# Kernel tuning notes

Hardware: AMD Instinct MI355X
Metric: run time of the kernel (lower is better)

The kernel has to match this reference:

```python
import jax, jax.numpy as jnp
import numpy as np

B, D, C, P, H, I, E, TOPK = 65536, 1024, 256, 32, 128, 32, 16, 2
FUSION = D + P  # 1056

def ln(x, g, b, eps=1e-5):
    m = jnp.mean(x, axis=-1, keepdims=True)
    v = jnp.mean((x - m) ** 2, axis=-1, keepdims=True)
    return (x - m) * jax.lax.rsqrt(v + eps) * g + b

def setup_inputs() -> dict:
    key = jax.random.key(0)
    ks = jax.random.split(key, 8)
    def w(k, shape):
        return jax.random.normal(k, shape, dtype=jnp.float32) * 0.02
    return {
        "x": jax.random.normal(ks[0], (B, D), dtype=jnp.float32),
        "context": jax.random.normal(ks[1], (B, C), dtype=jnp.float32),
        "en_g": jnp.ones((D,), jnp.float32), "en_b": jnp.zeros((D,), jnp.float32),
        "cn_g": jnp.ones((C,), jnp.float32), "cn_b": jnp.zeros((C,), jnp.float32),
        "cp1_w": w(ks[2], (C, P)), "cp1_b": jnp.zeros((P,), jnp.float32),
        "cp2_w": w(ks[3], (P, P)), "cp2_b": jnp.zeros((P,), jnp.float32),
        "cpn_g": jnp.ones((P,), jnp.float32), "cpn_b": jnp.zeros((P,), jnp.float32),
        "fn_g": jnp.ones((FUSION,), jnp.float32), "fn_b": jnp.zeros((FUSION,), jnp.float32),
        "gp1_w": w(ks[4], (FUSION, H)), "gp1_b": jnp.zeros((H,), jnp.float32),
        "ln1_g": jnp.ones((H,), jnp.float32), "ln1_b": jnp.zeros((H,), jnp.float32),
        "gp2_w": w(ks[5], (H, I)), "gp2_b": jnp.zeros((I,), jnp.float32),
        "ln2_g": jnp.ones((I,), jnp.float32), "ln2_b": jnp.zeros((I,), jnp.float32),
        "gp3_w": w(ks[6], (I, E)), "gp3_b": jnp.zeros((E,), jnp.float32),
    }

def reference(x, context, en_g, en_b, cn_g, cn_b, cp1_w, cp1_b, cp2_w, cp2_b,
              cpn_g, cpn_b, fn_g, fn_b, gp1_w, gp1_b, ln1_g, ln1_b,
              gp2_w, gp2_b, ln2_g, ln2_b, gp3_w, gp3_b):
    gelu = lambda t: jax.nn.gelu(t, approximate=False)  # torch default GELU (erf)
    emb = ln(x, en_g, en_b)                               # [B, D]
    ctx = ln(context, cn_g, cn_b)                         # [B, C]
    cf = gelu(ctx @ cp1_w + cp1_b) @ cp2_w + cp2_b        # [B, P]
    cf = ln(cf, cpn_g, cpn_b)
    fusion = ln(jnp.concatenate([emb, cf], axis=-1), fn_g, fn_b)  # [B, FUSION]
    h = gelu(ln(fusion @ gp1_w + gp1_b, ln1_g, ln1_b))    # [B, H]
    inter = gelu(ln(h @ gp2_w + gp2_b, ln2_g, ln2_b))     # [B, I]
    clean_logits = inter @ gp3_w + gp3_b                  # [B, E]
    # inference path: no noise injection (training=False)
    top_v, top_i = jax.lax.top_k(clean_logits, TOPK)
    combined_weights = jax.nn.softmax(top_v / 1.0, axis=-1)  # temperature=1.0
    return combined_weights, top_i, clean_logits
```

## Files before the change

### kernel.cpp

```cpp
#include <hip/hip_runtime.h>
#include <math.h>

namespace {

using s8v = __attribute__((ext_vector_type(8))) short;
using vf4 = __attribute__((ext_vector_type(4))) float;

constexpr int Bn = 65536;
constexpr int Rn = 64;

constexpr size_t OFF_A1H  = 0;
constexpr size_t OFF_A1M  = 270336;
constexpr size_t OFF_A1L  = 540672;
constexpr size_t OFF_C1H  = 811008;
constexpr size_t OFF_C1M  = 827392;
constexpr size_t OFF_C1L  = 843776;
constexpr size_t OFF_C2H  = 860160;
constexpr size_t OFF_C2M  = 862208;
constexpr size_t OFF_C2L  = 864256;
constexpr size_t OFF_G2H  = 866304;
constexpr size_t OFF_G2M  = 874496;
constexpr size_t OFF_G2L  = 882688;
constexpr size_t OFF_VPK  = 890880;
constexpr size_t OFF_UPK  = 892928;
constexpr size_t OFF_CST  = 893184;
constexpr size_t OFF_VPART= 893216;

__device__ __forceinline__ unsigned short bf16_rn(float f) {
    unsigned u = __float_as_uint(f);
    u += 0x7FFFu + ((u >> 16) & 1u);
    return (unsigned short)(u >> 16);
}
__device__ __forceinline__ float bf16_tof(unsigned short h) {
    return __uint_as_float(((unsigned)h) << 16);
}

union S8U { s8v v; unsigned short u[8]; };
union S8P { s8v v; unsigned u32[4]; };

__device__ __forceinline__ vf4 MFMA(s8v a, s8v b, vf4 c) {
    return __builtin_amdgcn_mfma_f32_16x16x32_bf16(a, b, c, 0, 0, 0);
}

__device__ __forceinline__ void mfma6(vf4& acc, s8v ah, s8v am, s8v al,
                                      s8v bh, s8v bm, s8v bl) {
    acc = MFMA(ah, bh, acc);
    acc = MFMA(ah, bm, acc);
    acc = MFMA(am, bh, acc);
    acc = MFMA(ah, bl, acc);
    acc = MFMA(al, bh, acc);
    acc = MFMA(am, bm, acc);
}

__device__ __forceinline__ void split3(float v, unsigned short& h,
                                       unsigned short& m, unsigned short& l) {
    h = bf16_rn(v);
    const float r = v - bf16_tof(h);
    m = bf16_rn(r);
    const float r2 = r - bf16_tof(m);
    l = bf16_rn(r2);
}

__device__ __forceinline__ void split3x8(const float* vv, s8v& H, s8v& M, s8v& L) {
    S8P h, m, l;
    #pragma unroll
    for (int p = 0; p < 4; ++p) {
        const float lo = vv[2 * p], hi = vv[2 * p + 1];
        unsigned ph, pm, pl;
        asm("v_cvt_pk_bf16_f32 %0, %1, %2" : "=v"(ph) : "v"(lo), "v"(hi));
        const float rlo = lo - __uint_as_float(ph << 16);
        const float rhi = hi - __uint_as_float(ph & 0xFFFF0000u);
        asm("v_cvt_pk_bf16_f32 %0, %1, %2" : "=v"(pm) : "v"(rlo), "v"(rhi));
        const float slo = rlo - __uint_as_float(pm << 16);
        const float shi = rhi - __uint_as_float(pm & 0xFFFF0000u);
        asm("v_cvt_pk_bf16_f32 %0, %1, %2" : "=v"(pl) : "v"(slo), "v"(shi));
        h.u32[p] = ph; m.u32[p] = pm; l.u32[p] = pl;
    }
    H = h.v; M = m.v; L = l.v;
}

__device__ __forceinline__ float gelu_f(float v) {
    return 0.5f * v * (1.0f + erff(v * 0.70710678118654752440f));
}

__device__ __forceinline__ void red16(float& s) {
    s += __shfl_xor(s, 1, 64); s += __shfl_xor(s, 2, 64);
    s += __shfl_xor(s, 4, 64); s += __shfl_xor(s, 8, 64);
}

__global__ void cag_prek1(const float* __restrict__ gp1_w,
                          const float* __restrict__ en_g, const float* __restrict__ en_b,
                          const float* __restrict__ fn_g, const float* __restrict__ fn_b,
                          char* __restrict__ ws)
{
    const int t = threadIdx.x, ch = blockIdx.x;
    s8v* A1h = (s8v*)(ws + OFF_A1H);
    s8v* A1m = (s8v*)(ws + OFF_A1M);
    s8v* A1l = (s8v*)(ws + OFF_A1L);
    float* Vpart = (float*)(ws + OFF_VPART);

    for (int s = t; s < 512; s += 256) {
        const int nt = s >> 6, lane = s & 63;
        const int n = nt * 16 + (lane & 15);
        const int jb = ch * 32 + 8 * (lane >> 4);
        S8U h, m, lo;
        #pragma unroll
        for (int r = 0; r < 8; ++r) {
            const int j = jb + r;
            const float sc = fn_g[j] * (j < 1024 ? en_g[j] : 1.0f);
            const float a = sc * gp1_w[(size_t)j * 128 + n];
            split3(a, h.u[r], m.u[r], lo.u[r]);
        }
        A1h[(ch * 8 + nt) * 64 + lane] = h.v;
        A1m[(ch * 8 + nt) * 64 + lane] = m.v;
        A1l[(ch * 8 + nt) * 64 + lane] = lo.v;
    }
    if (t < 128) {
        float v1 = 0.f, v2 = 0.f, v3 = 0.f, v4 = 0.f;
        for (int jj = 0; jj < 32; ++jj) {
            const int j = ch * 32 + jj;
            const float wv = gp1_w[(size_t)j * 128 + t];
            const float fg = fn_g[j];
            if (j < 1024) { v1 = fmaf(fg * en_g[j], wv, v1); v2 = fmaf(fg * en_b[j], wv, v2); }
            v3 = fmaf(fg, wv, v3);
            v4 = fmaf(fn_b[j], wv, v4);
        }
        float* p = Vpart + ((size_t)ch * 128 + t) * 4;
        p[0] = v1; p[1] = v2; p[2] = v3; p[3] = v4;
    }
}

__global__ void cag_prek2(const float* __restrict__ en_g, const float* __restrict__ en_b,
                          const float* __restrict__ cn_g, const float* __restrict__ cn_b,
                          const float* __restrict__ cp1_w, const float* __restrict__ cp1_b,
                          const float* __restrict__ cp2_w, const float* __restrict__ gp2_w,
                          const float* __restrict__ gp1_b,
                          char* __restrict__ ws)
{
    const int t = threadIdx.x, b = blockIdx.x;
    if (b == 0) {
        const float* Vpart = (const float*)(ws + OFF_VPART);
        float* Vpk = (float*)(ws + OFF_VPK);
        float* cst = (float*)(ws + OFF_CST);
        if (t < 128) {
            float v1 = 0.f, v2 = 0.f, v3 = 0.f, v4 = 0.f;
            for (int ch = 0; ch < 33; ++ch) {
                const float* p = Vpart + ((size_t)ch * 128 + t) * 4;
                v1 += p[0]; v2 += p[1]; v3 += p[2]; v4 += p[3];
            }
            v4 += gp1_b[t];
            float* q = Vpk + t * 4;
            q[0] = v1; q[1] = v2; q[2] = v3; q[3] = v4;
        }
        __shared__ float red[256];
        float part[5] = {0.f, 0.f, 0.f, 0.f, 0.f};
        for (int i = t; i < 1024; i += 256) {
            const float g = en_g[i], bb = en_b[i];
            part[0] += g; part[1] += bb; part[2] += g * g; part[3] += g * bb; part[4] += bb * bb;
        }
        for (int f = 0; f < 5; ++f) {
            red[t] = part[f]; __syncthreads();
            for (int s = 128; s > 0; s >>= 1) { if (t < s) red[t] += red[t + s]; __syncthreads(); }
            if (t == 0) cst[f] = red[0];
            __syncthreads();
        }
    } else if (b == 1) {
        s8v* C1h = (s8v*)(ws + OFF_C1H);
        s8v* C1m = (s8v*)(ws + OFF_C1M);
        s8v* C1l = (s8v*)(ws + OFF_C1L);
        float* up = (float*)(ws + OFF_UPK);
        for (int s = t; s < 8 * 2 * 64; s += 256) {
            const int ks = s >> 7, nt = (s >> 6) & 1, lane = s & 63;
            const int n = nt * 16 + (lane & 15);
            const int kb = ks * 32 + 8 * (lane >> 4);
            S8U h, m, lo;
            #pragma unroll
            for (int r = 0; r < 8; ++r) {
                const int k = kb + r;
                const float a = cn_g[k] * cp1_w[k * 32 + n];
                split3(a, h.u[r], m.u[r], lo.u[r]);
            }
            C1h[(ks * 2 + nt) * 64 + lane] = h.v;
            C1m[(ks * 2 + nt) * 64 + lane] = m.v;
            C1l[(ks * 2 + nt) * 64 + lane] = lo.v;
        }
        if (t < 32) {
            float u1 = 0.f, u2 = 0.f;
            for (int c = 0; c < 256; ++c) {
                u1 = fmaf(cn_g[c], cp1_w[c * 32 + t], u1);
                u2 = fmaf(cn_b[c], cp1_w[c * 32 + t], u2);
            }
            up[2 * t] = u1; up[2 * t + 1] = u2 + cp1_b[t];
        }
    } else if (b == 2) {
        s8v* C2h = (s8v*)(ws + OFF_C2H);
        s8v* C2m = (s8v*)(ws + OFF_C2M);
        s8v* C2l = (s8v*)(ws + OFF_C2L);
        if (t < 128) {
            const int nt = t >> 6, lane = t & 63;
            const int n = nt * 16 + (lane & 15);
            const int kb = 8 * (lane >> 4);
            S8U h, m, lo;
            #pragma unroll
            for (int r = 0; r < 8; ++r) {
                const float a = cp2_w[(kb + r) * 32 + n];
                split3(a, h.u[r], m.u[r], lo.u[r]);
            }
            C2h[nt * 64 + lane] = h.v;
            C2m[nt * 64 + lane] = m.v;
            C2l[nt * 64 + lane] = lo.v;
        }
    } else {
        s8v* G2h = (s8v*)(ws + OFF_G2H);
        s8v* G2m = (s8v*)(ws + OFF_G2M);
        s8v* G2l = (s8v*)(ws + OFF_G2L);
        for (int s = t; s < 4 * 2 * 64; s += 256) {
            const int ks = s >> 7, nt = (s >> 6) & 1, lane = s & 63;
            const int n = nt * 16 + (lane & 15);
            const int kb = ks * 32 + 8 * (lane >> 4);
            S8U h, m, lo;
            #pragma unroll
            for (int r = 0; r < 8; ++r) {
                const float a = gp2_w[(kb + r) * 32 + n];
                split3(a, h.u[r], m.u[r], lo.u[r]);
            }
            G2h[(ks * 2 + nt) * 64 + lane] = h.v;
            G2m[(ks * 2 + nt) * 64 + lane] = m.v;
            G2l[(ks * 2 + nt) * 64 + lane] = lo.v;
        }
    }
}

__global__ __launch_bounds__(256, 4)
void cag_main(const float* __restrict__ x, const float* __restrict__ ctx,
              const float* __restrict__ en_g, const float* __restrict__ en_b,
              const float* __restrict__ cpn_g, const float* __restrict__ cpn_b,
              const float* __restrict__ cp2_b,
              const float* __restrict__ ln1_g, const float* __restrict__ ln1_b,
              const float* __restrict__ gp2_b,
              const float* __restrict__ ln2_g, const float* __restrict__ ln2_b,
              const float* __restrict__ gp3_w, const float* __restrict__ gp3_b,
              const char* __restrict__ ws, float* __restrict__ out)
{
    __shared__ __attribute__((aligned(16))) char smU[64 * 132 * 4];
    __shared__ float s_sc4[64][4];
    __shared__ float part_s[4][64];
    __shared__ float part_s2[4][64];
    __shared__ float s_ln1[64][2];
    __shared__ float s_cfs[64], s_cfs2[64];

    short (*fragA)[4][64][8] = (short(*)[4][64][8])smU;
    float (*cfnbuf)[36] = (float(*)[36])(smU + 12288);
    float (*pbuf)[36]   = (float(*)[36])smU;
    float (*hbuf)[132]  = (float(*)[132])smU;
    float (*ibuf)[36]   = (float(*)[36])smU;
    float (*lbuf)[20]   = (float(*)[20])(smU + 16384);

    const int tid = threadIdx.x;
    const int l = tid & 63, w = tid >> 6;
    const int sg = l >> 4, lr = l & 15;
    const int row0 = blockIdx.x * Rn;

    const s8v* A1h = (const s8v*)(ws + OFF_A1H);
    const s8v* A1m = (const s8v*)(ws + OFF_A1M);
    const s8v* A1l = (const s8v*)(ws + OFF_A1L);
    const s8v* C1h = (const s8v*)(ws + OFF_C1H);
    const s8v* C1m = (const s8v*)(ws + OFF_C1M);
    const s8v* C1l = (const s8v*)(ws + OFF_C1L);
    const s8v* C2h = (const s8v*)(ws + OFF_C2H);
    const s8v* C2m = (const s8v*)(ws + OFF_C2M);
    const s8v* C2l = (const s8v*)(ws + OFF_C2L);
    const s8v* G2h = (const s8v*)(ws + OFF_G2H);
    const s8v* G2m = (const s8v*)(ws + OFF_G2M);
    const s8v* G2l = (const s8v*)(ws + OFF_G2L);
    const float* Vpk = (const float*)(ws + OFF_VPK);
    const float* upk = (const float*)(ws + OFF_UPK);
    const float* cst = (const float*)(ws + OFF_CST);

    {
        const int crow = row0 + 16 * w + lr;
        const float* cb = ctx + (size_t)crow * 256 + 8 * sg;
        float cs = 0.f, cs2 = 0.f;
        vf4 ac0 = {0.f, 0.f, 0.f, 0.f}, ac1 = {0.f, 0.f, 0.f, 0.f};
        #pragma unroll
        for (int ks = 0; ks < 8; ++ks) {
            const float4 a0 = *(const float4*)(cb + ks * 32);
            const float4 a1 = *(const float4*)(cb + ks * 32 + 4);
            const float vv[8] = {a0.x, a0.y, a0.z, a0.w, a1.x, a1.y, a1.z, a1.w};
            #pragma unroll
            for (int j = 0; j < 8; ++j) { cs += vv[j]; cs2 = fmaf(vv[j], vv[j], cs2); }
            s8v ah, am, al;
            split3x8(vv, ah, am, al);
            mfma6(ac0, ah, am, al,
                  C1h[(ks * 2 + 0) * 64 + l], C1m[(ks * 2 + 0) * 64 + l], C1l[(ks * 2 + 0) * 64 + l]);
            mfma6(ac1, ah, am, al,
                  C1h[(ks * 2 + 1) * 64 + l], C1m[(ks * 2 + 1) * 64 + l], C1l[(ks * 2 + 1) * 64 + l]);
        }
        cs += __shfl_xor(cs, 16, 64); cs += __shfl_xor(cs, 32, 64);
        cs2 += __shfl_xor(cs2, 16, 64); cs2 += __shfl_xor(cs2, 32, 64);
        const float cm = cs * (1.f / 256.f);
        const float crr = rsqrtf(cs2 * (1.f / 256.f) - cm * cm + 1e-5f);
        float m_r[4], r_r[4];
        #pragma unroll
        for (int rg = 0; rg < 4; ++rg) {
            const int src = 4 * sg + rg;
            m_r[rg] = __shfl(cm, src, 64);
            r_r[rg] = __shfl(crr, src, 64);
        }
        #pragma unroll
        for (int ntl = 0; ntl < 2; ++ntl) {
            const int c = 16 * ntl + lr;
            const float u1 = upk[2 * c], u2 = upk[2 * c + 1];
            #pragma unroll
            for (int rg = 0; rg < 4; ++rg) {
                const float av = (ntl == 0) ? ac0[rg] : ac1[rg];
                const float a1v = r_r[rg] * av - r_r[rg] * m_r[rg] * u1 + u2;
                pbuf[16 * w + 4 * sg + rg][c] = gelu_f(a1v);
            }
        }
        __syncthreads();
        float pv[8];
        const int prow = 16 * w + lr;
        *(float4*)&pv[0] = *(const float4*)&pbuf[prow][8 * sg];
        *(float4*)&pv[4] = *(const float4*)&pbuf[prow][8 * sg + 4];
        s8v ph, pm_, pl;
        split3x8(pv, ph, pm_, pl);
        vf4 a20 = {0.f, 0.f, 0.f, 0.f}, a21 = {0.f, 0.f, 0.f, 0.f};
        mfma6(a20, ph, pm_, pl, C2h[0 * 64 + l], C2m[0 * 64 + l], C2l[0 * 64 + l]);
        mfma6(a21, ph, pm_, pl, C2h[1 * 64 + l], C2m[1 * 64 + l], C2l[1 * 64 + l]);
        const float cb0 = cp2_b[lr], cb1 = cp2_b[16 + lr];
        const float cg0 = cpn_g[lr], cg1 = cpn_g[16 + lr];
        const float cbb0 = cpn_b[lr], cbb1 = cpn_b[16 + lr];
        __syncthreads();
        #pragma unroll
        for (int rg = 0; rg < 4; ++rg) {
            const float v0 = a20[rg] + cb0, v1 = a21[rg] + cb1;
            float s = v0 + v1, s2 = v0 * v0 + v1 * v1;
            red16(s); red16(s2);
            const float pm = s * (1.f / 32.f);
            const float prs = rsqrtf(s2 * (1.f / 32.f) - pm * pm + 1e-5f);
            const float cn0 = (v0 - pm) * prs * cg0 + cbb0;
            const float cn1 = (v1 - pm) * prs * cg1 + cbb1;
            float t = cn0 + cn1, t2 = cn0 * cn0 + cn1 * cn1;
            red16(t); red16(t2);
            const int rr = 16 * w + 4 * sg + rg;
            if (lr == 0) { s_cfs[rr] = t; s_cfs2[rr] = t2; }
            cfnbuf[rr][lr] = cn0; cfnbuf[rr][16 + lr] = cn1;
        }
    }
    __syncthreads();

    vf4 acc[4][2];
    #pragma unroll
    for (int mt = 0; mt < 4; ++mt) { acc[mt][0] = vf4{0.f,0.f,0.f,0.f}; acc[mt][1] = vf4{0.f,0.f,0.f,0.f}; }

    float Sx = 0.f, Sxx = 0.f, Sxg = 0.f, Sxg2 = 0.f, Sxgb = 0.f, Sq = 0.f;

    const float* xb = x + (size_t)(row0 + 16 * w + lr) * 1024 + 8 * sg;
    const int nt0 = 2 * w;

    float4 xc0 = *(const float4*)(xb);
    float4 xc1 = *(const float4*)(xb + 4);
    float4 xn0, xn1;

    #pragma unroll 1
    for (int ks = 0; ks <= 32; ++ks) {
        const size_t q = (size_t)((ks * 8 + nt0) * 64 + l);
        const s8v B0h = A1h[q],      B0m = A1m[q],      B0l = A1l[q];
        const s8v B1h = A1h[q + 64], B1m = A1m[q + 64], B1l = A1l[q + 64];
        if (ks < 31) {
            xn0 = *(const float4*)(xb + (ks + 1) * 32);
            xn1 = *(const float4*)(xb + (ks + 1) * 32 + 4);
        }
        if (ks < 32) {
            const int kb = ks * 32 + 8 * sg;
            const float4 g0 = *(const float4*)(en_g + kb);
            const float4 g1 = *(const float4*)(en_g + kb + 4);
            const float4 e0 = *(const float4*)(en_b + kb);
            const float4 e1 = *(const float4*)(en_b + kb + 4);
            const float vv[8] = {xc0.x, xc0.y, xc0.z, xc0.w, xc1.x, xc1.y, xc1.z, xc1.w};
            const float gg[8] = {g0.x, g0.y, g0.z, g0.w, g1.x, g1.y, g1.z, g1.w};
            const float ee[8] = {e0.x, e0.y, e0.z, e0.w, e1.x, e1.y, e1.z, e1.w};
            #pragma unroll
            for (int j = 0; j < 8; ++j) {
                const float v = vv[j], g = gg[j], b = ee[j];
                Sx += v; Sxx = fmaf(v, v, Sxx);
                const float t = v * g;
                Sxg += t; Sxg2 = fmaf(t, g, Sxg2); Sxgb = fmaf(t, b, Sxgb); Sq = fmaf(t, t, Sq);
            }
            s8v H, M, L;
            split3x8(vv, H, M, L);
            *(s8v*)&fragA[0][w][l][0] = H;
            *(s8v*)&fragA[1][w][l][0] = M;
            *(s8v*)&fragA[2][w][l][0] = L;
        } else {
            float sx = Sx, sxx = Sxx, sxg = Sxg, sxg2 = Sxg2, sxgb = Sxgb, sq = Sq;
            #define RED2(s) { s += __shfl_xor(s, 16, 64); s += __shfl_xor(s, 32, 64); }
            RED2(sx) RED2(sxx) RED2(sxg) RED2(sxg2) RED2(sxgb) RED2(sq)
            #undef RED2
            const float xm = sx * (1.f / 1024.f);
            const float xvar = sxx * (1.f / 1024.f) - xm * xm;
            const float xr = rsqrtf(xvar + 1e-5f);
            const float xrinv = sqrtf(xvar + 1e-5f);
            const float Gs = cst[0], Bs = cst[1], Sg2c = cst[2], Sgbc = cst[3], Sb2c = cst[4];
            const float Semb = xr * (sxg - xm * Gs) + Bs;
            const float Semb2 = xr * xr * (sq - 2.f * xm * sxg2 + xm * xm * Sg2c)
                              + 2.f * xr * (sxgb - xm * Sgbc) + Sb2c;
            const int rr = 16 * w + lr;
            const float fm = (Semb + s_cfs[rr]) * (1.f / 1056.f);
            const float fvar = (Semb2 + s_cfs2[rr]) * (1.f / 1056.f) - fm * fm;
            const float fr = rsqrtf(fvar + 1e-5f);
            if (sg == 0) {
                s_sc4[rr][0] = fr * xr; s_sc4[rr][1] = -fr * xr * xm;
                s_sc4[rr][2] = fr;      s_sc4[rr][3] = -fr * fm;
            }
            float vv[8];
            *(float4*)&vv[0] = *(const float4*)&cfnbuf[rr][8 * sg];
            *(float4*)&vv[4] = *(const float4*)&cfnbuf[rr][8 * sg + 4];
            #pragma unroll
            for (int j = 0; j < 8; ++j) vv[j] *= xrinv;
            s8v H, M, L;
            split3x8(vv, H, M, L);
            *(s8v*)&fragA[0][w][l][0] = H;
            *(s8v*)&fragA[1][w][l][0] = M;
            *(s8v*)&fragA[2][w][l][0] = L;
        }
        asm volatile("s_waitcnt lgkmcnt(0)\n\ts_barrier" ::: "memory");

        __builtin_amdgcn_s_setprio(1);
        #pragma unroll
        for (int mt = 0; mt < 4; ++mt) {
            const s8v ah = *(const s8v*)&fragA[0][mt][l][0];
            const s8v am = *(const s8v*)&fragA[1][mt][l][0];
            const s8v al = *(const s8v*)&fragA[2][mt][l][0];
            mfma6(acc[mt][0], ah, am, al, B0h, B0m, B0l);
            mfma6(acc[mt][1], ah, am, al, B1h, B1m, B1l);
        }
        __builtin_amdgcn_s_setprio(0);
        asm volatile("s_barrier" ::: "memory");
        xc0 = xn0; xc1 = xn1;
    }

    {
        const int tc0 = 16 * (2 * w) + lr, tc1 = 16 * (2 * w + 1) + lr;
        float4 Vc[2];
        Vc[0] = *(const float4*)&Vpk[tc0 * 4];
        Vc[1] = *(const float4*)&Vpk[tc1 * 4];
        #pragma unroll
        for (int mt = 0; mt < 4; ++mt) {
            #pragma unroll
            for (int rg = 0; rg < 4; ++rg) {
                const float4 sc = *(const float4*)&s_sc4[16 * mt + 4 * sg + rg][0];
                #pragma unroll
                for (int ntl = 0; ntl < 2; ++ntl) {
                    acc[mt][ntl][rg] = sc.x * acc[mt][ntl][rg] + sc.y * Vc[ntl].x
                                     + sc.z * Vc[ntl].y + sc.w * Vc[ntl].z + Vc[ntl].w;
                }
            }
        }
        #pragma unroll
        for (int mt = 0; mt < 4; ++mt) {
            #pragma unroll
            for (int rg = 0; rg < 4; ++rg) {
                const float v0 = acc[mt][0][rg], v1 = acc[mt][1][rg];
                float s = v0 + v1, s2 = v0 * v0 + v1 * v1;
                red16(s); red16(s2);
                if (lr == 0) {
                    const int rr = 16 * mt + 4 * sg + rg;
                    part_s[w][rr] = s; part_s2[w][rr] = s2;
                }
            }
        }
        __syncthreads();
        if (tid < 64) {
            const float s = part_s[0][tid] + part_s[1][tid] + part_s[2][tid] + part_s[3][tid];
            const float s2 = part_s2[0][tid] + part_s2[1][tid] + part_s2[2][tid] + part_s2[3][tid];
            const float mn = s * (1.f / 128.f);
            s_ln1[tid][0] = mn;
            s_ln1[tid][1] = rsqrtf(s2 * (1.f / 128.f) - mn * mn + 1e-5f);
        }
        __syncthreads();
        float g1c[2], b1c[2];
        g1c[0] = ln1_g[tc0]; b1c[0] = ln1_b[tc0];
        g1c[1] = ln1_g[tc1]; b1c[1] = ln1_b[tc1];
        #pragma unroll
        for (int mt = 0; mt < 4; ++mt) {
            #pragma unroll
            for (int rg = 0; rg < 4; ++rg) {
                const int rr = 16 * mt + 4 * sg + rg;
                const float mn = s_ln1[rr][0], rs = s_ln1[rr][1];
                #pragma unroll
                for (int ntl = 0; ntl < 2; ++ntl) {
                    const float hp = gelu_f((acc[mt][ntl][rg] - mn) * rs * g1c[ntl] + b1c[ntl]);
                    hbuf[rr][16 * (2 * w + ntl) + lr] = hp;
                }
            }
        }
        __syncthreads();
    }

    float iv[2][4];
    {
        vf4 aG0 = {0.f, 0.f, 0.f, 0.f}, aG1 = {0.f, 0.f, 0.f, 0.f};
        const int hrow = 16 * w + lr;
        #pragma unroll
        for (int ks = 0; ks < 4; ++ks) {
            float pv[8];
            *(float4*)&pv[0] = *(const float4*)&hbuf[hrow][ks * 32 + 8 * sg];
            *(float4*)&pv[4] = *(const float4*)&hbuf[hrow][ks * 32 + 8 * sg + 4];
            s8v ah, am, al;
            split3x8(pv, ah, am, al);
            mfma6(aG0, ah, am, al,
                  G2h[(ks * 2 + 0) * 64 + l], G2m[(ks * 2 + 0) * 64 + l], G2l[(ks * 2 + 0) * 64 + l]);
            mfma6(aG1, ah, am, al,
                  G2h[(ks * 2 + 1) * 64 + l], G2m[(ks * 2 + 1) * 64 + l], G2l[(ks * 2 + 1) * 64 + l]);
        }
        const float gb0 = gp2_b[lr], gb1 = gp2_b[16 + lr];
        const float lg0 = ln2_g[lr], lg1 = ln2_g[16 + lr];
        const float lb0 = ln2_b[lr], lb1 = ln2_b[16 + lr];
        #pragma unroll
        for (int rg = 0; rg < 4; ++rg) {
            const float v0 = aG0[rg] + gb0, v1 = aG1[rg] + gb1;
            float s = v0 + v1, s2 = v0 * v0 + v1 * v1;
            red16(s); red16(s2);
            const float mn = s * (1.f / 32.f);
            const float rs = rsqrtf(s2 * (1.f / 32.f) - mn * mn + 1e-5f);
            iv[0][rg] = gelu_f((v0 - mn) * rs * lg0 + lb0);
            iv[1][rg] = gelu_f((v1 - mn) * rs * lg1 + lb1);
        }
    }
    __syncthreads();
    #pragma unroll
    for (int rg = 0; rg < 4; ++rg) {
        const int rr = 16 * w + 4 * sg + rg;
        ibuf[rr][lr] = iv[0][rg];
        ibuf[rr][16 + lr] = iv[1][rg];
    }
    __syncthreads();

    {
        const int r = tid >> 2, e4 = (tid & 3) * 4;
        float a0 = 0.f, a1 = 0.f, a2 = 0.f, a3 = 0.f;
        #pragma unroll 4
        for (int qq = 0; qq < 32; ++qq) {
            const float v = ibuf[r][qq];
            const float4 w3 = *(const float4*)(gp3_w + qq * 16 + e4);
            a0 = fmaf(v, w3.x, a0); a1 = fmaf(v, w3.y, a1);
            a2 = fmaf(v, w3.z, a2); a3 = fmaf(v, w3.w, a3);
        }
        const float4 b3 = *(const float4*)(gp3_b + e4);
        const float4 lg = make_float4(a0 + b3.x, a1 + b3.y, a2 + b3.z, a3 + b3.w);
        float* outl = out + (size_t)Bn * 4;
        *(float4*)(outl + (size_t)(row0 + r) * 16 + e4) = lg;
        *(float4*)&lbuf[r][e4] = lg;
    }
    __syncthreads();
    if (tid < 64) {
        float v[16];
        #pragma unroll
        for (int e = 0; e < 4; ++e) *(float4*)&v[e * 4] = *(const float4*)&lbuf[tid][e * 4];
        int i0 = 0; float v0 = v[0];
        #pragma unroll
        for (int e = 1; e < 16; ++e) if (v[e] > v0) { v0 = v[e]; i0 = e; }
        int i1 = -1; float v1 = -3.4e38f;
        #pragma unroll
        for (int e = 0; e < 16; ++e) if (e != i0 && v[e] > v1) { v1 = v[e]; i1 = e; }
        const float e1 = expf(v1 - v0);
        const float inv = 1.0f / (1.0f + e1);
        const size_t g = (size_t)(row0 + tid);
        out[g * 2 + 0] = inv;
        out[g * 2 + 1] = e1 * inv;
        float* outi = out + (size_t)Bn * 2;
        outi[g * 2 + 0] = (float)i0;
        outi[g * 2 + 1] = (float)i1;
    }
}

}

extern "C" void kernel_launch(void* const* d_in, const int* in_sizes, int n_in,
                              void* d_out, int out_size, void* d_ws, size_t ws_size,
                              hipStream_t stream) {
    const float* x     = (const float*)d_in[0];
    const float* ctx   = (const float*)d_in[1];
    const float* en_g  = (const float*)d_in[2];
    const float* en_b  = (const float*)d_in[3];
    const float* cn_g  = (const float*)d_in[4];
    const float* cn_b  = (const float*)d_in[5];
    const float* cp1_w = (const float*)d_in[6];
    const float* cp1_b = (const float*)d_in[7];
    const float* cp2_w = (const float*)d_in[8];
    const float* cp2_b = (const float*)d_in[9];
    const float* cpn_g = (const float*)d_in[10];
    const float* cpn_b = (const float*)d_in[11];
    const float* fn_g  = (const float*)d_in[12];
    const float* fn_b  = (const float*)d_in[13];
    const float* gp1_w = (const float*)d_in[14];
    const float* gp1_b = (const float*)d_in[15];
    const float* ln1_g = (const float*)d_in[16];
    const float* ln1_b = (const float*)d_in[17];
    const float* gp2_w = (const float*)d_in[18];
    const float* gp2_b = (const float*)d_in[19];
    const float* ln2_g = (const float*)d_in[20];
    const float* ln2_b = (const float*)d_in[21];
    const float* gp3_w = (const float*)d_in[22];
    const float* gp3_b = (const float*)d_in[23];

    char* ws = (char*)d_ws;
    hipLaunchKernelGGL(cag_prek1, dim3(33), dim3(256), 0, stream,
                       gp1_w, en_g, en_b, fn_g, fn_b, ws);
    hipLaunchKernelGGL(cag_prek2, dim3(4), dim3(256), 0, stream,
                       en_g, en_b, cn_g, cn_b, cp1_w, cp1_b, cp2_w, gp2_w, gp1_b, ws);
    hipLaunchKernelGGL(cag_main, dim3(Bn / Rn), dim3(256), 0, stream,
                       x, ctx, en_g, en_b, cpn_g, cpn_b, cp2_b,
                       ln1_g, ln1_b, gp2_b, ln2_g, ln2_b, gp3_w, gp3_b,
                       ws, (float*)d_out);
}
```

Before: 194.6 us.

## Process two K-steps per barrier pair in first GEMM main loop

Unrolls the fused LayerNorm plus split-bf16 GEMM loop so each iteration stages two 32-wide K slices into a doubled LDS fragment buffer. This halves the number of barrier pairs and gives more MFMA work between synchronisations. The final context-feature K step is peeled out of the loop. In exchange it uses more LDS, which moves cfnbuf, and needs more registers for the extra B fragments and x prefetches, which may cut occupancy under launch_bounds(256,4).

```diff
diff --git a/kernel.cpp b/kernel.cpp
--- a/kernel.cpp
+++ b/kernel.cpp
@@ -249,8 +249,8 @@
     __shared__ float s_ln1[64][2];
     __shared__ float s_cfs[64], s_cfs2[64];
 
-    short (*fragA)[4][64][8] = (short(*)[4][64][8])smU;
-    float (*cfnbuf)[36] = (float(*)[36])(smU + 12288);
+    short (*fragA)[3][4][64][8] = (short(*)[3][4][64][8])smU;
+    float (*cfnbuf)[36] = (float(*)[36])(smU + 24576);
     float (*pbuf)[36]   = (float(*)[36])smU;
     float (*hbuf)[132]  = (float(*)[132])smU;
     float (*ibuf)[36]   = (float(*)[36])smU;
@@ -359,28 +359,35 @@
     const float* xb = x + (size_t)(row0 + 16 * w + lr) * 1024 + 8 * sg;
     const int nt0 = 2 * w;
 
-    float4 xc0 = *(const float4*)(xb);
-    float4 xc1 = *(const float4*)(xb + 4);
-    float4 xn0, xn1;
+    float4 xc0a = *(const float4*)(xb);
+    float4 xc0b = *(const float4*)(xb + 4);
+    float4 xc1a = *(const float4*)(xb + 32);
+    float4 xc1b = *(const float4*)(xb + 36);
+    float4 xn0a, xn0b, xn1a, xn1b;
 
     #pragma unroll 1
-    for (int ks = 0; ks <= 32; ++ks) {
-        const size_t q = (size_t)((ks * 8 + nt0) * 64 + l);
-        const s8v B0h = A1h[q],      B0m = A1m[q],      B0l = A1l[q];
-        const s8v B1h = A1h[q + 64], B1m = A1m[q + 64], B1l = A1l[q + 64];
-        if (ks < 31) {
-            xn0 = *(const float4*)(xb + (ks + 1) * 32);
-            xn1 = *(const float4*)(xb + (ks + 1) * 32 + 4);
-        }
-        if (ks < 32) {
-            const int kb = ks * 32 + 8 * sg;
-            const float4 g0 = *(const float4*)(en_g + kb);
-            const float4 g1 = *(const float4*)(en_g + kb + 4);
-            const float4 e0 = *(const float4*)(en_b + kb);
-            const float4 e1 = *(const float4*)(en_b + kb + 4);
-            const float vv[8] = {xc0.x, xc0.y, xc0.z, xc0.w, xc1.x, xc1.y, xc1.z, xc1.w};
-            const float gg[8] = {g0.x, g0.y, g0.z, g0.w, g1.x, g1.y, g1.z, g1.w};
-            const float ee[8] = {e0.x, e0.y, e0.z, e0.w, e1.x, e1.y, e1.z, e1.w};
+    for (int p = 0; p < 16; ++p) {
+        const int k0 = 2 * p, k1 = 2 * p + 1;
+        const size_t q0 = (size_t)((k0 * 8 + nt0) * 64 + l);
+        const s8v B00h = A1h[q0],      B00m = A1m[q0],      B00l = A1l[q0];
+        const s8v B01h = A1h[q0 + 64], B01m = A1m[q0 + 64], B01l = A1l[q0 + 64];
+        const size_t q1 = (size_t)((k1 * 8 + nt0) * 64 + l);
+        const s8v B10h = A1h[q1],      B10m = A1m[q1],      B10l = A1l[q1];
+        const s8v B11h = A1h[q1 + 64], B11m = A1m[q1 + 64], B11l = A1l[q1 + 64];
+        const int kb0 = k0 * 32 + 8 * sg, kb1 = k1 * 32 + 8 * sg;
+        const float4 g00 = *(const float4*)(en_g + kb0);
+        const float4 g01 = *(const float4*)(en_g + kb0 + 4);
+        const float4 e00 = *(const float4*)(en_b + kb0);
+        const float4 e01 = *(const float4*)(en_b + kb0 + 4);
+        const float4 g10 = *(const float4*)(en_g + kb1);
+        const float4 g11 = *(const float4*)(en_g + kb1 + 4);
+        const float4 e10 = *(const float4*)(en_b + kb1);
+        const float4 e11 = *(const float4*)(en_b + kb1 + 4);
+
+        {
+            const float vv[8] = {xc0a.x, xc0a.y, xc0a.z, xc0a.w, xc0b.x, xc0b.y, xc0b.z, xc0b.w};
+            const float gg[8] = {g00.x, g00.y, g00.z, g00.w, g01.x, g01.y, g01.z, g01.w};
+            const float ee[8] = {e00.x, e00.y, e00.z, e00.w, e01.x, e01.y, e01.z, e01.w};
             #pragma unroll
             for (int j = 0; j < 8; ++j) {
                 const float v = vv[j], g = gg[j], b = ee[j];
@@ -390,55 +397,103 @@
             }
             s8v H, M, L;
             split3x8(vv, H, M, L);
-            *(s8v*)&fragA[0][w][l][0] = H;
-            *(s8v*)&fragA[1][w][l][0] = M;
-            *(s8v*)&fragA[2][w][l][0] = L;
-        } else {
-            float sx = Sx, sxx = Sxx, sxg = Sxg, sxg2 = Sxg2, sxgb = Sxgb, sq = Sq;
-            #define RED2(s) { s += __shfl_xor(s, 16, 64); s += __shfl_xor(s, 32, 64); }
-            RED2(sx) RED2(sxx) RED2(sxg) RED2(sxg2) RED2(sxgb) RED2(sq)
-            #undef RED2
-            const float xm = sx * (1.f / 1024.f);
-            const float xvar = sxx * (1.f / 1024.f) - xm * xm;
-            const float xr = rsqrtf(xvar + 1e-5f);
-            const float xrinv = sqrtf(xvar + 1e-5f);
-            const float Gs = cst[0], Bs = cst[1], Sg2c = cst[2], Sgbc = cst[3], Sb2c = cst[4];
-            const float Semb = xr * (sxg - xm * Gs) + Bs;
-            const float Semb2 = xr * xr * (sq - 2.f * xm * sxg2 + xm * xm * Sg2c)
-                              + 2.f * xr * (sxgb - xm * Sgbc) + Sb2c;
-            const int rr = 16 * w + lr;
-            const float fm = (Semb + s_cfs[rr]) * (1.f / 1056.f);
-            const float fvar = (Semb2 + s_cfs2[rr]) * (1.f / 1056.f) - fm * fm;
-            const float fr = rsqrtf(fvar + 1e-5f);
-            if (sg == 0) {
-                s_sc4[rr][0] = fr * xr; s_sc4[rr][1] = -fr * xr * xm;
-                s_sc4[rr][2] = fr;      s_sc4[rr][3] = -fr * fm;
-            }
-            float vv[8];
-            *(float4*)&vv[0] = *(const float4*)&cfnbuf[rr][8 * sg];
-            *(float4*)&vv[4] = *(const float4*)&cfnbuf[rr][8 * sg + 4];
-            #pragma unroll
-            for (int j = 0; j < 8; ++j) vv[j] *= xrinv;
+            *(s8v*)&fragA[0][0][w][l][0] = H;
+            *(s8v*)&fragA[0][1][w][l][0] = M;
+            *(s8v*)&fragA[0][2][w][l][0] = L;
+        }
+        {
+            const float vv[8] = {xc1a.x, xc1a.y, xc1a.z, xc1a.w, xc1b.x, xc1b.y, xc1b.z, xc1b.w};
+            const float gg[8] = {g10.x, g10.y, g10.z, g10.w, g11.x, g11.y, g11.z, g11.w};
+            const float ee[8] = {e10.x, e10.y, e10.z, e10.w, e11.x, e11.y, e11.z, e11.w};
+            #pragma unroll
+            for (int j = 0; j < 8; ++j) {
+                const float v = vv[j], g = gg[j], b = ee[j];
+                Sx += v; Sxx = fmaf(v, v, Sxx);
+                const float t = v * g;
+                Sxg += t; Sxg2 = fmaf(t, g, Sxg2); Sxgb = fmaf(t, b, Sxgb); Sq = fmaf(t, t, Sq);
+            }
             s8v H, M, L;
             split3x8(vv, H, M, L);
-            *(s8v*)&fragA[0][w][l][0] = H;
-            *(s8v*)&fragA[1][w][l][0] = M;
-            *(s8v*)&fragA[2][w][l][0] = L;
+            *(s8v*)&fragA[1][0][w][l][0] = H;
+            *(s8v*)&fragA[1][1][w][l][0] = M;
+            *(s8v*)&fragA[1][2][w][l][0] = L;
+        }
+        if (p < 15) {
+            xn0a = *(const float4*)(xb + (k0 + 2) * 32);
+            xn0b = *(const float4*)(xb + (k0 + 2) * 32 + 4);
+            xn1a = *(const float4*)(xb + (k1 + 2) * 32);
+            xn1b = *(const float4*)(xb + (k1 + 2) * 32 + 4);
         }
         asm volatile("s_waitcnt lgkmcnt(0)\n\ts_barrier" ::: "memory");
 
         __builtin_amdgcn_s_setprio(1);
         #pragma unroll
         for (int mt = 0; mt < 4; ++mt) {
-            const s8v ah = *(const s8v*)&fragA[0][mt][l][0];
-            const s8v am = *(const s8v*)&fragA[1][mt][l][0];
-            const s8v al = *(const s8v*)&fragA[2][mt][l][0];
-            mfma6(acc[mt][0], ah, am, al, B0h, B0m, B0l);
-            mfma6(acc[mt][1], ah, am, al, B1h, B1m, B1l);
+            const s8v ah = *(const s8v*)&fragA[0][0][mt][l][0];
+            const s8v am = *(const s8v*)&fragA[0][1][mt][l][0];
+            const s8v al = *(const s8v*)&fragA[0][2][mt][l][0];
+            mfma6(acc[mt][0], ah, am, al, B00h, B00m, B00l);
+            mfma6(acc[mt][1], ah, am, al, B01h, B01m, B01l);
+        }
+        #pragma unroll
+        for (int mt = 0; mt < 4; ++mt) {
+            const s8v ah = *(const s8v*)&fragA[1][0][mt][l][0];
+            const s8v am = *(const s8v*)&fragA[1][1][mt][l][0];
+            const s8v al = *(const s8v*)&fragA[1][2][mt][l][0];
+            mfma6(acc[mt][0], ah, am, al, B10h, B10m, B10l);
+            mfma6(acc[mt][1], ah, am, al, B11h, B11m, B11l);
         }
         __builtin_amdgcn_s_setprio(0);
         asm volatile("s_barrier" ::: "memory");
-        xc0 = xn0; xc1 = xn1;
+        xc0a = xn0a; xc0b = xn0b; xc1a = xn1a; xc1b = xn1b;
+    }
+
+    {
+        const size_t qf = (size_t)((32 * 8 + nt0) * 64 + l);
+        const s8v Bfh0 = A1h[qf],      Bfm0 = A1m[qf],      Bfl0 = A1l[qf];
+        const s8v Bfh1 = A1h[qf + 64], Bfm1 = A1m[qf + 64], Bfl1 = A1l[qf + 64];
+
+        float sx = Sx, sxx = Sxx, sxg = Sxg, sxg2 = Sxg2, sxgb = Sxgb, sq = Sq;
+        #define RED2(s) { s += __shfl_xor(s, 16, 64); s += __shfl_xor(s, 32, 64); }
+        RED2(sx) RED2(sxx) RED2(sxg) RED2(sxg2) RED2(sxgb) RED2(sq)
+        #undef RED2
+        const float xm = sx * (1.f / 1024.f);
+        const float xvar = sxx * (1.f / 1024.f) - xm * xm;
+        const float xr = rsqrtf(xvar + 1e-5f);
+        const float xrinv = sqrtf(xvar + 1e-5f);
+        const float Gs = cst[0], Bs = cst[1], Sg2c = cst[2], Sgbc = cst[3], Sb2c = cst[4];
+        const float Semb = xr * (sxg - xm * Gs) + Bs;
+        const float Semb2 = xr * xr * (sq - 2.f * xm * sxg2 + xm * xm * Sg2c)
+                          + 2.f * xr * (sxgb - xm * Sgbc) + Sb2c;
+        const int rr = 16 * w + lr;
+        const float fm = (Semb + s_cfs[rr]) * (1.f / 1056.f);
+        const float fvar = (Semb2 + s_cfs2[rr]) * (1.f / 1056.f) - fm * fm;
+        const float fr = rsqrtf(fvar + 1e-5f);
+        if (sg == 0) {
+            s_sc4[rr][0] = fr * xr; s_sc4[rr][1] = -fr * xr * xm;
+            s_sc4[rr][2] = fr;      s_sc4[rr][3] = -fr * fm;
+        }
+        float vv[8];
+        *(float4*)&vv[0] = *(const float4*)&cfnbuf[rr][8 * sg];
+        *(float4*)&vv[4] = *(const float4*)&cfnbuf[rr][8 * sg + 4];
+        #pragma unroll
+        for (int j = 0; j < 8; ++j) vv[j] *= xrinv;
+        s8v H, M, L;
+        split3x8(vv, H, M, L);
+        *(s8v*)&fragA[0][0][w][l][0] = H;
+        *(s8v*)&fragA[0][1][w][l][0] = M;
+        *(s8v*)&fragA[0][2][w][l][0] = L;
+        asm volatile("s_waitcnt lgkmcnt(0)\n\ts_barrier" ::: "memory");
+        __builtin_amdgcn_s_setprio(1);
+        #pragma unroll
+        for (int mt = 0; mt < 4; ++mt) {
+            const s8v ah = *(const s8v*)&fragA[0][0][mt][l][0];
+            const s8v am = *(const s8v*)&fragA[0][1][mt][l][0];
+            const s8v al = *(const s8v*)&fragA[0][2][mt][l][0];
+            mfma6(acc[mt][0], ah, am, al, Bfh0, Bfm0, Bfl0);
+            mfma6(acc[mt][1], ah, am, al, Bfh1, Bfm1, Bfl1);
+        }
+        __builtin_amdgcn_s_setprio(0);
     }
 
     {
```

After: 407.6 us. +109.5%, slower.
